# Optimization experiments

Hardware: AMD Instinct MI355X
Metric: run time of the kernel (lower is better)

Reference implementation:

```python
import jax, jax.numpy as jnp
import numpy as np

N = 1048576        # number of time samples (rays)
V = 32             # num_videos
D = 32             # embedding_dim
F = 6              # num_frequencies
K = 2 * F + 1      # basis size: [1, sin(2^j*pi*t), cos(2^j*pi*t)]


def setup_inputs() -> dict:
    key = jax.random.key(0)
    k1, k2, k3 = jax.random.split(key, 3)
    times = jax.random.uniform(k1, (N, 1), dtype=jnp.float32)
    video_ids = jax.random.randint(k2, (N, 1), 0, V, dtype=jnp.int32)
    weights = jax.random.normal(k3, (V, D, K), dtype=jnp.float32)
    return {"times": times, "video_ids": video_ids, "weights": weights}


def _fourier_basis(t):
    # t: [N] -> [N, K] with basis [1, sin(2^j pi t), cos(2^j pi t)] j=0..F-1
    freqs = (2.0 ** jnp.arange(F, dtype=t.dtype)) * jnp.pi  # [F]
    ang = t[:, None] * freqs                                # [N, F]
    return jnp.concatenate(
        [jnp.ones_like(t)[:, None], jnp.sin(ang), jnp.cos(ang)], axis=-1
    )


def reference(times, video_ids, weights):
    shp = times.shape
    t = times.reshape(-1)                       # [N]
    vid = video_ids.reshape(-1).astype(jnp.int32)  # [N]
    basis = _fourier_basis(t)                   # [N, K]
    w = weights[vid]                            # gather: [N, D, K]
    emb = jnp.einsum('ndk,nk->nd', w, basis)    # [N, D]
    return emb.reshape((*shp[:-1], -1))
```

## Files before the change

kernel.cpp:

```cpp
#include <hip/hip_runtime.h>
#include <hip/hip_fp16.h>

#define NRAYS 1048576
#define NV 32
#define ND 32
#define NF 6
#define NK 13

typedef _Float16 h2 __attribute__((ext_vector_type(2)));
typedef float f4 __attribute__((ext_vector_type(4)));

__device__ __forceinline__ float fdot2acc(h2 a, h2 b, float c) {
#if __has_builtin(__builtin_amdgcn_fdot2)
    return __builtin_amdgcn_fdot2(a, b, c, false);
#else
    return c + (float)a.x * (float)b.x + (float)a.y * (float)b.y;
#endif
}

__device__ __forceinline__ h2 pack2(float a, float b) {
#if __has_builtin(__builtin_amdgcn_cvt_pkrtz)
    return __builtin_bit_cast(h2, __builtin_amdgcn_cvt_pkrtz(a, b));
#else
    h2 r; r.x = (_Float16)a; r.y = (_Float16)b; return r;
#endif
}

__device__ __forceinline__ float hwsin(float rev) {
#if __has_builtin(__builtin_amdgcn_sinf)
    return __builtin_amdgcn_sinf(rev);
#else
    return __sinf(6.28318530717958647692f * rev);
#endif
}
__device__ __forceinline__ float hwcos(float rev) {
#if __has_builtin(__builtin_amdgcn_cosf)
    return __builtin_amdgcn_cosf(rev);
#else
    return __cosf(6.28318530717958647692f * rev);
#endif
}

__global__ void pack_weights_kernel(const float* __restrict__ weights,
                                    unsigned* __restrict__ wpack)
{
    int j = blockIdx.x * 256 + threadIdx.x;
    if (j >= NV * 7 * 32) return;
    int v = j / 224;
    int r = j - v * 224;
    int i = r >> 5;
    int c = r & 31;
    int pos = c >> 2;
    int e = c & 3;
    int q = pos ^ (v & 7);
    int d = 4 * q + e;
    float w0 = weights[v * (ND * NK) + d * NK + 2 * i];
    float w1 = (2 * i + 1 < NK) ? weights[v * (ND * NK) + d * NK + 2 * i + 1] : 0.f;
    h2 p = pack2(w0, w1);
    wpack[j] = __builtin_bit_cast(unsigned, p);
}

__global__ __launch_bounds__(256, 5) void VideoEmbedding_kernel(
    const float* __restrict__ times,
    const int* __restrict__ vids,
    const unsigned* __restrict__ wpack,
    float* __restrict__ out)
{
    __shared__ _Float16 wl[NV * 7 * ND * 2];
    __shared__ int hist[NV];
    __shared__ float s_t[256];
    __shared__ int s_meta[256];

    const int tid = threadIdx.x;

    {
        const uint4* src = reinterpret_cast<const uint4*>(wpack);
        uint4* dst = reinterpret_cast<uint4*>(wl);
#pragma unroll
        for (int j = 0; j < 7; ++j)
            dst[tid + j * 256] = src[tid + j * 256];
    }

    const int q = tid & 7;
    const int g = tid >> 3;

    const int NCHUNK = NRAYS / 256;
    for (int chunk = blockIdx.x; chunk < NCHUNK; chunk += gridDim.x) {
        const int base = chunk * 256;
        const float t = times[base + tid];
        const int vid = vids[base + tid];

        if (tid < NV) hist[tid] = 0;
        __syncthreads();
        atomicAdd(&hist[vid], 1);
        __syncthreads();
        if (tid < NV) {
            int c = hist[tid];
            int sum = c;
#pragma unroll
            for (int off = 1; off < NV; off <<= 1) {
                int n = __shfl_up(sum, off, NV);
                if (tid >= off) sum += n;
            }
            hist[tid] = sum - c;
        }
        __syncthreads();
        {
            int pos = atomicAdd(&hist[vid], 1);
            s_t[pos] = t;
            s_meta[pos] = (vid << 8) | tid;
        }
        __syncthreads();

#pragma unroll 2
        for (int p = 0; p < 8; ++p) {
            const int slot = p * 32 + g;
            const float ts = s_t[slot];
            const int meta = s_meta[slot];
            const int v = meta >> 8;
            const int lidx = meta & 255;

            float sv[NF], cv[NF];
            sv[0] = hwsin(0.5f * ts);
            cv[0] = hwcos(0.5f * ts);
#pragma unroll
            for (int j = 1; j < NF; ++j) {
                float sj = sv[j - 1], cj = cv[j - 1];
                sv[j] = 2.f * sj * cj;
                cv[j] = fmaf(-2.f * sj, sj, 1.f);
            }

            h2 bp[7];
            bp[0] = pack2(1.0f, sv[0]);
            bp[1] = pack2(sv[1], sv[2]);
            bp[2] = pack2(sv[3], sv[4]);
            bp[3] = pack2(sv[5], cv[0]);
            bp[4] = pack2(cv[1], cv[2]);
            bp[5] = pack2(cv[3], cv[4]);
            bp[6] = pack2(cv[5], 0.0f);

            const unsigned posq = (unsigned)(q ^ (v & 7));
            const unsigned baddr = (unsigned)v * 448u + posq * 8u;
            float a0 = 0.f, a1 = 0.f, a2 = 0.f, a3 = 0.f;
#pragma unroll
            for (int i = 0; i < 7; ++i) {
                uint4 w = *reinterpret_cast<const uint4*>(&wl[baddr + i * 64]);
                a0 = fdot2acc(__builtin_bit_cast(h2, w.x), bp[i], a0);
                a1 = fdot2acc(__builtin_bit_cast(h2, w.y), bp[i], a1);
                a2 = fdot2acc(__builtin_bit_cast(h2, w.z), bp[i], a2);
                a3 = fdot2acc(__builtin_bit_cast(h2, w.w), bp[i], a3);
            }

            f4 res;
            res.x = a0; res.y = a1; res.z = a2; res.w = a3;
            __builtin_nontemporal_store(res,
                reinterpret_cast<f4*>(out) + (size_t)(base + lidx) * 8 + q);
        }
        __syncthreads();
    }
}

extern "C" void kernel_launch(void* const* d_in, const int* in_sizes, int n_in,
                              void* d_out, int out_size, void* d_ws, size_t ws_size,
                              hipStream_t stream) {
    const float* times = (const float*)d_in[0];
    const int* vids = (const int*)d_in[1];
    const float* weights = (const float*)d_in[2];
    float* out = (float*)d_out;
    unsigned* wpack = (unsigned*)d_ws;

    hipLaunchKernelGGL(pack_weights_kernel, dim3(28), dim3(256), 0, stream,
                       weights, wpack);
    hipLaunchKernelGGL(VideoEmbedding_kernel, dim3(1280), dim3(256), 0, stream,
                       times, vids, wpack, out);
}
```

Before: 39.07 us.

## Replace per-ray fdot2 contraction with MFMA tiles over video-sorted rays

Each block now takes 1024 rays and buckets them by video id. It builds fp16 basis rows in shared memory and breaks each video's bucket into 16-row tiles. Each wave then multiplies a tile by that video's weight fragments, loaded straight from global memory, using two 16x16x32 MFMA instructions. This swaps the per-ray dot2 loops for matrix cores and removes the per-block staging of all weights into shared memory. The costs are padded tiles, scattered scalar 4-byte output stores instead of 16-byte nontemporal stores, and lower occupancy (launch bounds cut from 5 to 4).

```diff
diff --git a/kernel.cpp b/kernel.cpp
--- a/kernel.cpp
+++ b/kernel.cpp
@@ -6,17 +6,12 @@
 #define ND 32
 #define NF 6
 #define NK 13
+#define RPB 1024
+#define NTILE_MAX 96
 
 typedef _Float16 h2 __attribute__((ext_vector_type(2)));
+typedef _Float16 h8 __attribute__((ext_vector_type(8)));
 typedef float f4 __attribute__((ext_vector_type(4)));
-
-__device__ __forceinline__ float fdot2acc(h2 a, h2 b, float c) {
-#if __has_builtin(__builtin_amdgcn_fdot2)
-    return __builtin_amdgcn_fdot2(a, b, c, false);
-#else
-    return c + (float)a.x * (float)b.x + (float)a.y * (float)b.y;
-#endif
-}
 
 __device__ __forceinline__ h2 pack2(float a, float b) {
 #if __has_builtin(__builtin_amdgcn_cvt_pkrtz)
@@ -25,7 +20,6 @@
     h2 r; r.x = (_Float16)a; r.y = (_Float16)b; return r;
 #endif
 }
-
 __device__ __forceinline__ float hwsin(float rev) {
 #if __has_builtin(__builtin_amdgcn_sinf)
     return __builtin_amdgcn_sinf(rev);
@@ -42,121 +36,142 @@
 }
 
 __global__ void pack_weights_kernel(const float* __restrict__ weights,
-                                    unsigned* __restrict__ wpack)
+                                    unsigned* __restrict__ wfrag)
 {
-    int j = blockIdx.x * 256 + threadIdx.x;
-    if (j >= NV * 7 * 32) return;
-    int v = j / 224;
-    int r = j - v * 224;
-    int i = r >> 5;
-    int c = r & 31;
-    int pos = c >> 2;
-    int e = c & 3;
-    int q = pos ^ (v & 7);
-    int d = 4 * q + e;
-    float w0 = weights[v * (ND * NK) + d * NK + 2 * i];
-    float w1 = (2 * i + 1 < NK) ? weights[v * (ND * NK) + d * NK + 2 * i + 1] : 0.f;
-    h2 p = pack2(w0, w1);
-    wpack[j] = __builtin_bit_cast(unsigned, p);
+    int idx = blockIdx.x * 256 + threadIdx.x;
+    if (idx >= 16384) return;
+    int v = idx >> 9;
+    int r = idx & 511;
+    int dhalf = r >> 8;
+    int r2 = r & 255;
+    int lane = r2 >> 2;
+    int e = r2 & 3;
+    int d = dhalf * 16 + (lane & 15);
+    int k0 = (lane >> 4) * 8 + 2 * e;
+    const float* wp = weights + v * (ND * NK) + d * NK;
+    float w0 = (k0 < NK) ? wp[k0] : 0.f;
+    float w1 = (k0 + 1 < NK) ? wp[k0 + 1] : 0.f;
+    wfrag[idx] = __builtin_bit_cast(unsigned, pack2(w0, w1));
 }
 
-__global__ __launch_bounds__(256, 5) void VideoEmbedding_kernel(
+__global__ __launch_bounds__(256, 4) void VideoEmbedding_kernel(
     const float* __restrict__ times,
     const int* __restrict__ vids,
-    const unsigned* __restrict__ wpack,
+    const uint4* __restrict__ wfrag,
     float* __restrict__ out)
 {
-    __shared__ _Float16 wl[NV * 7 * ND * 2];
+    __shared__ __align__(16) _Float16 s_bt[(RPB + 16) * 16];
+    __shared__ unsigned short s_meta[RPB];
     __shared__ int hist[NV];
-    __shared__ float s_t[256];
-    __shared__ int s_meta[256];
+    __shared__ unsigned ttab[NTILE_MAX];
+    __shared__ int s_nT;
 
     const int tid = threadIdx.x;
+    const int rbase = blockIdx.x * RPB;
 
-    {
-        const uint4* src = reinterpret_cast<const uint4*>(wpack);
-        uint4* dst = reinterpret_cast<uint4*>(wl);
+    if (tid < NV) hist[tid] = 0;
+    __syncthreads();
+
+    float t[4];
+    int v[4];
 #pragma unroll
-        for (int j = 0; j < 7; ++j)
-            dst[tid + j * 256] = src[tid + j * 256];
+    for (int it = 0; it < 4; ++it) {
+        int lid = it * 256 + tid;
+        t[it] = times[rbase + lid];
+        v[it] = vids[rbase + lid];
+        atomicAdd(&hist[v[it]], 1);
     }
+    __syncthreads();
 
-    const int q = tid & 7;
-    const int g = tid >> 3;
+    if (tid < NV) {
+        int c = hist[tid];
+        int sum = c;
+#pragma unroll
+        for (int off = 1; off < NV; off <<= 1) {
+            int n = __shfl_up(sum, off, NV);
+            if (tid >= off) sum += n;
+        }
+        int excl = sum - c;
+        hist[tid] = excl;
+        int nt = (c + 15) >> 4;
+        int tsum = nt;
+#pragma unroll
+        for (int off = 1; off < NV; off <<= 1) {
+            int n = __shfl_up(tsum, off, NV);
+            if (tid >= off) tsum += n;
+        }
+        int texcl = tsum - nt;
+        if (tid == NV - 1) s_nT = tsum;
+        unsigned endv = (unsigned)(excl + c);
+        for (int s = 0; s < nt; ++s)
+            ttab[texcl + s] =
+                ((unsigned)tid << 22) | (endv << 11) | (unsigned)(excl + 16 * s);
+        uint4 zz; zz.x = zz.y = zz.z = zz.w = 0u;
+        *reinterpret_cast<uint4*>(&s_bt[RPB * 16 + tid * 8]) = zz;
+    }
+    __syncthreads();
 
-    const int NCHUNK = NRAYS / 256;
-    for (int chunk = blockIdx.x; chunk < NCHUNK; chunk += gridDim.x) {
-        const int base = chunk * 256;
-        const float t = times[base + tid];
-        const int vid = vids[base + tid];
+#pragma unroll
+    for (int it = 0; it < 4; ++it) {
+        int slot = atomicAdd(&hist[v[it]], 1);
+        s_meta[slot] = (unsigned short)(it * 256 + tid);
+        float sv[NF], cv[NF];
+        sv[0] = hwsin(0.5f * t[it]);
+        cv[0] = hwcos(0.5f * t[it]);
+#pragma unroll
+        for (int j = 1; j < NF; ++j) {
+            float sj = sv[j - 1], cj = cv[j - 1];
+            sv[j] = 2.f * sj * cj;
+            cv[j] = fmaf(-2.f * sj, sj, 1.f);
+        }
+        uint4 lo, hi;
+        lo.x = __builtin_bit_cast(unsigned, pack2(1.0f, sv[0]));
+        lo.y = __builtin_bit_cast(unsigned, pack2(sv[1], sv[2]));
+        lo.z = __builtin_bit_cast(unsigned, pack2(sv[3], sv[4]));
+        lo.w = __builtin_bit_cast(unsigned, pack2(sv[5], cv[0]));
+        hi.x = __builtin_bit_cast(unsigned, pack2(cv[1], cv[2]));
+        hi.y = __builtin_bit_cast(unsigned, pack2(cv[3], cv[4]));
+        hi.z = __builtin_bit_cast(unsigned, pack2(cv[5], 0.0f));
+        hi.w = 0u;
+        uint4* bt = reinterpret_cast<uint4*>(&s_bt[slot * 16]);
+        bt[0] = lo;
+        bt[1] = hi;
+    }
+    __syncthreads();
 
-        if (tid < NV) hist[tid] = 0;
-        __syncthreads();
-        atomicAdd(&hist[vid], 1);
-        __syncthreads();
-        if (tid < NV) {
-            int c = hist[tid];
-            int sum = c;
+    const int wid = tid >> 6;
+    const int lane = tid & 63;
+    const int lrow = lane & 15;
+    const int lkc = lane >> 4;
+    const int T = s_nT;
+
+    for (int tt = wid; tt < T; tt += 4) {
+        const unsigned e = ttab[tt];
+        const int rowstart = (int)(e & 0x7FFu);
+        const int rend = (int)((e >> 11) & 0x7FFu);
+        const int vv = (int)(e >> 22);
+
+        h8 a = *reinterpret_cast<const h8*>(
+            &s_bt[(rowstart + lrow) * 16 + lkc * 8]);
+        uint4 b0u = wfrag[(vv * 2 + 0) * 64 + lane];
+        uint4 b1u = wfrag[(vv * 2 + 1) * 64 + lane];
+
+        f4 z = {0.f, 0.f, 0.f, 0.f};
+        f4 c0 = __builtin_amdgcn_mfma_f32_16x16x32_f16(
+            a, __builtin_bit_cast(h8, b0u), z, 0, 0, 0);
+        f4 c1 = __builtin_amdgcn_mfma_f32_16x16x32_f16(
+            a, __builtin_bit_cast(h8, b1u), z, 0, 0, 0);
+
 #pragma unroll
-            for (int off = 1; off < NV; off <<= 1) {
-                int n = __shfl_up(sum, off, NV);
-                if (tid >= off) sum += n;
+        for (int j = 0; j < 4; ++j) {
+            const int srow = rowstart + lkc * 4 + j;
+            if (srow < rend) {
+                const int lidx = s_meta[srow];
+                float* o = out + (size_t)(rbase + lidx) * 32 + lrow;
+                o[0] = c0[j];
+                o[16] = c1[j];
             }
-            hist[tid] = sum - c;
         }
-        __syncthreads();
-        {
-            int pos = atomicAdd(&hist[vid], 1);
-            s_t[pos] = t;
-            s_meta[pos] = (vid << 8) | tid;
-        }
-        __syncthreads();
-
-#pragma unroll 2
-        for (int p = 0; p < 8; ++p) {
-            const int slot = p * 32 + g;
-            const float ts = s_t[slot];
-            const int meta = s_meta[slot];
-            const int v = meta >> 8;
-            const int lidx = meta & 255;
-
-            float sv[NF], cv[NF];
-            sv[0] = hwsin(0.5f * ts);
-            cv[0] = hwcos(0.5f * ts);
-#pragma unroll
-            for (int j = 1; j < NF; ++j) {
-                float sj = sv[j - 1], cj = cv[j - 1];
-                sv[j] = 2.f * sj * cj;
-                cv[j] = fmaf(-2.f * sj, sj, 1.f);
-            }
-
-            h2 bp[7];
-            bp[0] = pack2(1.0f, sv[0]);
-            bp[1] = pack2(sv[1], sv[2]);
-            bp[2] = pack2(sv[3], sv[4]);
-            bp[3] = pack2(sv[5], cv[0]);
-            bp[4] = pack2(cv[1], cv[2]);
-            bp[5] = pack2(cv[3], cv[4]);
-            bp[6] = pack2(cv[5], 0.0f);
-
-            const unsigned posq = (unsigned)(q ^ (v & 7));
-            const unsigned baddr = (unsigned)v * 448u + posq * 8u;
-            float a0 = 0.f, a1 = 0.f, a2 = 0.f, a3 = 0.f;
-#pragma unroll
-            for (int i = 0; i < 7; ++i) {
-                uint4 w = *reinterpret_cast<const uint4*>(&wl[baddr + i * 64]);
-                a0 = fdot2acc(__builtin_bit_cast(h2, w.x), bp[i], a0);
-                a1 = fdot2acc(__builtin_bit_cast(h2, w.y), bp[i], a1);
-                a2 = fdot2acc(__builtin_bit_cast(h2, w.z), bp[i], a2);
-                a3 = fdot2acc(__builtin_bit_cast(h2, w.w), bp[i], a3);
-            }
-
-            f4 res;
-            res.x = a0; res.y = a1; res.z = a2; res.w = a3;
-            __builtin_nontemporal_store(res,
-                reinterpret_cast<f4*>(out) + (size_t)(base + lidx) * 8 + q);
-        }
-        __syncthreads();
     }
 }
 
@@ -167,10 +182,10 @@
     const int* vids = (const int*)d_in[1];
     const float* weights = (const float*)d_in[2];
     float* out = (float*)d_out;
-    unsigned* wpack = (unsigned*)d_ws;
+    unsigned* wfrag = (unsigned*)d_ws;
 
-    hipLaunchKernelGGL(pack_weights_kernel, dim3(28), dim3(256), 0, stream,
-                       weights, wpack);
-    hipLaunchKernelGGL(VideoEmbedding_kernel, dim3(1280), dim3(256), 0, stream,
-                       times, vids, wpack, out);
+    hipLaunchKernelGGL(pack_weights_kernel, dim3(64), dim3(256), 0, stream,
+                       weights, wfrag);
+    hipLaunchKernelGGL(VideoEmbedding_kernel, dim3(1024), dim3(256), 0, stream,
+                       times, vids, (const uint4*)wfrag, out);
 }
```

Measured after the change: 36.75 us. 1.06x faster.
